# Kernel optimization log

Hardware: AMD Instinct MI355X
Metric: run time of the kernel (lower is better)

The kernel has to match this reference:

```python
import jax, jax.numpy as jnp
import numpy as np

WS = 8          # window_size
HEADS = 6
DH = 32         # dim_head


def _dwconv(t, w):
    # t: (B,C,H,W), w: (C,1,3,3) depthwise, stride 1, padding 1 -> SAME
    return jax.lax.conv_general_dilated(
        t, w, window_strides=(1, 1), padding='SAME',
        feature_group_count=t.shape[1],
        dimension_numbers=('NCHW', 'OIHW', 'NCHW'))


def _l2norm(t, eps=1e-12):
    # matches F.normalize: x / max(||x||, eps)
    n = jnp.sqrt(jnp.sum(t * t, axis=-1, keepdims=True))
    return t / jnp.maximum(n, eps)


def setup_inputs() -> dict:
    key = jax.random.key(0)
    ks = jax.random.split(key, 10)
    B, H, W, C = 2, 256, 256, 192
    s = 0.05
    return {
        'x': jax.random.normal(ks[0], (B, H, W, C), jnp.float32),
        'illu_fea_trans': jax.random.normal(ks[1], (B, H, W, C), jnp.float32),
        'gt_w': jax.random.normal(ks[2], (C, C), jnp.float32) * s,
        'gt_b': jax.random.normal(ks[3], (C,), jnp.float32) * s,
        'qkv_w': jax.random.normal(ks[4], (C, 3 * C), jnp.float32) * s,
        'qkv_b': jax.random.normal(ks[5], (3 * C,), jnp.float32) * s,
        'proj_w': jax.random.normal(ks[6], (C, C), jnp.float32) * s,
        'proj_b': jax.random.normal(ks[7], (C,), jnp.float32) * s,
        'conv1_w': jax.random.normal(ks[8], (C, 1, 3, 3), jnp.float32) * s,
        'conv2_w': jax.random.normal(ks[9], (C, 1, 3, 3), jnp.float32) * s,
    }


def reference(x, illu_fea_trans, gt_w, gt_b, qkv_w, qkv_b, proj_w, proj_b,
              conv1_w, conv2_w):
    B, H, W, C = x.shape
    Ws, heads, d = WS, HEADS, DH
    scale = d ** (-0.5)
    pad_h = (Ws - H % Ws) % Ws
    pad_w = (Ws - W % Ws) % Ws
    xp = jnp.pad(x, ((0, 0), (0, pad_h), (0, pad_w), (0, 0)), mode='reflect')
    ip = jnp.pad(illu_fea_trans, ((0, 0), (0, pad_h), (0, pad_w), (0, 0)), mode='reflect')
    Hp, Wp = xp.shape[1], xp.shape[2]
    nW = (Hp // Ws) * (Wp // Ws)
    T = Ws * Ws

    def to_windows(t):
        t = t.reshape(B, Hp // Ws, Ws, Wp // Ws, Ws, C)
        return t.transpose(0, 1, 3, 2, 4, 5).reshape(B * nW, T, C)

    xw = to_windows(xp)                                  # (B*nW, T, C)
    qkv = (xw @ qkv_w + qkv_b).reshape(B * nW, T, 3, heads, d)
    qkv = qkv.transpose(2, 0, 3, 1, 4)                   # (3, Bn, h, T, d)
    q, k, v = qkv[0], qkv[1], qkv[2]
    q = _l2norm(q)
    k = _l2norm(k)

    illu = to_windows(ip).reshape(B * nW, T, heads, d).transpose(0, 2, 1, 3)
    v = v * (1.0 + jax.nn.sigmoid(illu))

    # global token: avg-pool over padded spatial dims, then linear
    gt = jnp.mean(xp, axis=(1, 2)) @ gt_w + gt_b          # (B, C)
    gt = gt.reshape(B, heads, 1, d)
    # faithful to torch expand(dim=2 -> nW).reshape(B*nW, heads, 1, d)
    gk = jnp.broadcast_to(gt, (B, heads, nW, d)).reshape(B * nW, heads, 1, d)
    k = jnp.concatenate([k, gk], axis=2)                  # (Bn, h, T+1, d)
    v = jnp.concatenate([v, gk], axis=2)

    # chunked softmax over keys == full softmax over key axis (chunks on q only)
    attn = jax.nn.softmax(jnp.einsum('bhqd,bhkd->bhqk', q, k) * scale, axis=-1)
    out = jnp.einsum('bhqk,bhkd->bhqd', attn, v)          # (Bn, h, T, d)
    out = out.transpose(0, 2, 1, 3).reshape(B * nW, T, C)
    out = out @ proj_w + proj_b

    out = out.reshape(B, Hp // Ws, Wp // Ws, Ws, Ws, C)
    out = out.transpose(0, 1, 3, 2, 4, 5).reshape(B, Hp, Wp, C)[:, :H, :W, :]

    # depthwise-conv positional branch on padded x (exact gelu like torch)
    t = xp.transpose(0, 3, 1, 2)                          # (B,C,Hp,Wp)
    t = _dwconv(t, conv1_w)
    t = jax.nn.gelu(t, approximate=False)
    t = _dwconv(t, conv2_w)
    pos = t.transpose(0, 2, 3, 1)[:, :H, :W, :]
    return out + pos
```

## Files before the change

kernel.cpp:

```cpp
#include <hip/hip_runtime.h>
#include <hip/hip_bf16.h>

#define BB   2
#define HH   256
#define WWD  256
#define CC   192
#define WSZ  8
#define TT   64
#define NHD  6
#define DHD  32
#define N3   576

typedef __attribute__((ext_vector_type(8))) short short8;
typedef __attribute__((ext_vector_type(4))) float f32x4;

__device__ inline short bf16_bits(float f) {
  __hip_bfloat16 h = __float2bfloat16(f);
  return __builtin_bit_cast(short, h);
}

__global__ __launch_bounds__(256) void lcam_wshuf(const float* __restrict__ src,
                                                  short* __restrict__ dst,
                                                  int ncols, int nfrag) {
  int gid = blockIdx.x * 256 + threadIdx.x;
  if (gid >= nfrag) return;
  int lane = gid & 63;
  int s = (gid >> 6) % 6;
  int ct = gid / 384;
  int col = ct * 16 + (lane & 15);
  int k0 = s * 32 + (lane >> 4) * 8;
  short8 v;
#pragma unroll
  for (int j = 0; j < 8; ++j)
    v[j] = bf16_bits(src[(size_t)(k0 + j) * ncols + col]);
  *(short8*)(dst + (size_t)gid * 8) = v;
}

__global__ __launch_bounds__(256) void lcam_sum_x(const float* __restrict__ x,
                                                  float* __restrict__ sums) {
  int blk = blockIdx.x;
  int b = blk >> 9;
  int chunk = blk & 511;
  const float* xp = x + ((size_t)b * 65536 + (size_t)chunk * 128) * CC;
  int t = threadIdx.x;
  if (t < CC) {
    float acc = 0.f;
    for (int p = 0; p < 128; ++p) acc += xp[(size_t)p * CC + t];
    atomicAdd(&sums[b * CC + t], acc);
  }
}

__global__ void lcam_gt(const float* __restrict__ sums,
                        const float* __restrict__ gt_w,
                        const float* __restrict__ gt_b,
                        float* __restrict__ gt) {
  int b = blockIdx.x;
  int co = threadIdx.x;
  float acc = gt_b[co];
  const float inv = 1.f / 65536.f;
  for (int c = 0; c < CC; ++c)
    acc += sums[b * CC + c] * inv * gt_w[c * CC + co];
  gt[b * CC + co] = acc;
}

__global__ __launch_bounds__(256) void lcam_attn(
    const float* __restrict__ x, const float* __restrict__ illu,
    const short* __restrict__ wf, const short* __restrict__ pwf,
    const float* __restrict__ qkv_b, const float* __restrict__ proj_b,
    const float* __restrict__ gt, float* __restrict__ out) {
  __shared__ __align__(16) short qs[64 * 40];
  __shared__ __align__(16) short ks[2][65 * 40];
  __shared__ __align__(16) short vt[2][32 * 72];
  __shared__ __align__(16) short ps[64 * 72];
  __shared__ __align__(16) short ot[64 * 40];

  int w = blockIdx.x;
  int b  = w >> 10;
  int wy = (w >> 5) & 31;
  int wx = w & 31;
  int t  = threadIdx.x;
  int lane = t & 63;
  int rtile = t >> 6;
  int m = lane & 15;
  int quad = lane >> 4;
  int key0 = rtile * 16 + quad * 4;

  size_t base = ((size_t)(b * HH + wy * WSZ) * WWD + wx * WSZ) * CC;

  int apix = rtile * 16 + m;
  size_t arow = base + (size_t)((apix >> 3) * WWD + (apix & 7)) * CC + quad * 8;
  short8 afrag[6];
#pragma unroll
  for (int s = 0; s < 6; ++s) {
    const float* ap = x + arow + s * 32;
    float4 f0 = *(const float4*)(ap);
    float4 f1 = *(const float4*)(ap + 4);
    short8 v;
    v[0] = bf16_bits(f0.x); v[1] = bf16_bits(f0.y);
    v[2] = bf16_bits(f0.z); v[3] = bf16_bits(f0.w);
    v[4] = bf16_bits(f1.x); v[5] = bf16_bits(f1.y);
    v[6] = bf16_bits(f1.z); v[7] = bf16_bits(f1.w);
    afrag[s] = v;
  }
  const short8* wf8 = (const short8*)wf;
  const short8* pwf8 = (const short8*)pwf;

  f32x4 pacc[12];
#pragma unroll
  for (int ct = 0; ct < 12; ++ct) {
    f32x4 z = {0.f, 0.f, 0.f, 0.f};
    pacc[ct] = z;
  }

  for (int h = 0; h < NHD; ++h) {
    short* ksb = ks[h & 1];
    short* vtb = vt[h & 1];
    float gv0 = gt[b * CC + h * 32 + m];
    float gv1 = gt[b * CC + h * 32 + 16 + m];
    float il0[4], il1[4];
#pragma unroll
    for (int r = 0; r < 4; ++r) {
      int key = key0 + r;
      const float* ip = illu + base + (size_t)((key >> 3) * WWD + (key & 7)) * CC + h * 32;
      il0[r] = ip[m];
      il1[r] = ip[16 + m];
    }
    {
      f32x4 a0 = {0.f,0.f,0.f,0.f}, a1 = {0.f,0.f,0.f,0.f};
      __builtin_amdgcn_s_setprio(1);
#pragma unroll
      for (int s = 0; s < 6; ++s)
        a0 = __builtin_amdgcn_mfma_f32_16x16x32_bf16(afrag[s], wf8[(2*h)*384 + s*64 + lane], a0, 0,0,0);
#pragma unroll
      for (int s = 0; s < 6; ++s)
        a1 = __builtin_amdgcn_mfma_f32_16x16x32_bf16(afrag[s], wf8[(2*h+1)*384 + s*64 + lane], a1, 0,0,0);
      __builtin_amdgcn_s_setprio(0);
      float b0 = qkv_b[h*32 + m], b1 = qkv_b[h*32 + 16 + m];
#pragma unroll
      for (int r = 0; r < 4; ++r) {
        float v0 = a0[r] + b0, v1 = a1[r] + b1;
        float ss = v0*v0 + v1*v1;
        ss += __shfl_xor(ss, 1); ss += __shfl_xor(ss, 2);
        ss += __shfl_xor(ss, 4); ss += __shfl_xor(ss, 8);
        float scl = 0.17677669529663688f * __builtin_amdgcn_rsqf(fmaxf(ss, 1e-24f));
        int row = key0 + r;
        qs[row*40 + m]      = bf16_bits(v0 * scl);
        qs[row*40 + 16 + m] = bf16_bits(v1 * scl);
      }
    }
    {
      f32x4 a0 = {0.f,0.f,0.f,0.f}, a1 = {0.f,0.f,0.f,0.f};
      __builtin_amdgcn_s_setprio(1);
#pragma unroll
      for (int s = 0; s < 6; ++s)
        a0 = __builtin_amdgcn_mfma_f32_16x16x32_bf16(afrag[s], wf8[(12+2*h)*384 + s*64 + lane], a0, 0,0,0);
#pragma unroll
      for (int s = 0; s < 6; ++s)
        a1 = __builtin_amdgcn_mfma_f32_16x16x32_bf16(afrag[s], wf8[(13+2*h)*384 + s*64 + lane], a1, 0,0,0);
      __builtin_amdgcn_s_setprio(0);
      float b0 = qkv_b[192 + h*32 + m], b1 = qkv_b[192 + h*32 + 16 + m];
#pragma unroll
      for (int r = 0; r < 4; ++r) {
        float v0 = a0[r] + b0, v1 = a1[r] + b1;
        float ss = v0*v0 + v1*v1;
        ss += __shfl_xor(ss, 1); ss += __shfl_xor(ss, 2);
        ss += __shfl_xor(ss, 4); ss += __shfl_xor(ss, 8);
        float scl = __builtin_amdgcn_rsqf(fmaxf(ss, 1e-24f));
        int row = key0 + r;
        ksb[row*40 + m]      = bf16_bits(v0 * scl);
        ksb[row*40 + 16 + m] = bf16_bits(v1 * scl);
      }
    }
    {
      f32x4 a0 = {0.f,0.f,0.f,0.f}, a1 = {0.f,0.f,0.f,0.f};
      __builtin_amdgcn_s_setprio(1);
#pragma unroll
      for (int s = 0; s < 6; ++s)
        a0 = __builtin_amdgcn_mfma_f32_16x16x32_bf16(afrag[s], wf8[(24+2*h)*384 + s*64 + lane], a0, 0,0,0);
#pragma unroll
      for (int s = 0; s < 6; ++s)
        a1 = __builtin_amdgcn_mfma_f32_16x16x32_bf16(afrag[s], wf8[(25+2*h)*384 + s*64 + lane], a1, 0,0,0);
      __builtin_amdgcn_s_setprio(0);
      float b0 = qkv_b[384 + h*32 + m], b1 = qkv_b[384 + h*32 + 16 + m];
#pragma unroll
      for (int r = 0; r < 4; ++r) {
        int key = key0 + r;
        float s0 = __builtin_amdgcn_rcpf(1.f + __expf(-il0[r]));
        float s1 = __builtin_amdgcn_rcpf(1.f + __expf(-il1[r]));
        vtb[m*72 + key]        = bf16_bits((a0[r] + b0) * (1.f + s0));
        vtb[(16 + m)*72 + key] = bf16_bits((a1[r] + b1) * (1.f + s1));
      }
    }
    if (t < DHD) ksb[64*40 + t] = bf16_bits(gt[b*CC + h*DHD + t]);
    __syncthreads();
    short8 qa = *(const short8*)(qs + (rtile*16 + m)*40 + quad*8);
    f32x4 sc[5];
#pragma unroll
    for (int ct = 0; ct < 4; ++ct) {
      short8 kb = *(const short8*)(ksb + (ct*16 + m)*40 + quad*8);
      f32x4 z = {0.f,0.f,0.f,0.f};
      sc[ct] = __builtin_amdgcn_mfma_f32_16x16x32_bf16(qa, kb, z, 0,0,0);
    }
    {
      short8 kb = *(const short8*)(ksb + 64*40 + quad*8);
      f32x4 z = {0.f,0.f,0.f,0.f};
      sc[4] = __builtin_amdgcn_mfma_f32_16x16x32_bf16(qa, kb, z, 0,0,0);
    }
    float p64v[4], invr[4];
#pragma unroll
    for (int r = 0; r < 4; ++r) {
      float e0 = __expf(sc[0][r]), e1 = __expf(sc[1][r]);
      float e2 = __expf(sc[2][r]), e3 = __expf(sc[3][r]);
      float e4 = (m == 0) ? __expf(sc[4][r]) : 0.f;
      int row = key0 + r;
      ps[row*72 + m]      = bf16_bits(e0);
      ps[row*72 + 16 + m] = bf16_bits(e1);
      ps[row*72 + 32 + m] = bf16_bits(e2);
      ps[row*72 + 48 + m] = bf16_bits(e3);
      float sum = e0 + e1 + e2 + e3 + e4;
      sum += __shfl_xor(sum, 1); sum += __shfl_xor(sum, 2);
      sum += __shfl_xor(sum, 4); sum += __shfl_xor(sum, 8);
      invr[r] = __builtin_amdgcn_rcpf(sum);
      p64v[r] = e4;
    }
    f32x4 o0 = {0.f,0.f,0.f,0.f}, o1 = {0.f,0.f,0.f,0.f};
    __builtin_amdgcn_s_setprio(1);
#pragma unroll
    for (int kc = 0; kc < 2; ++kc) {
      short8 pa  = *(const short8*)(ps + (rtile*16 + m)*72 + kc*32 + quad*8);
      short8 vb0 = *(const short8*)(vtb + m*72        + kc*32 + quad*8);
      short8 vb1 = *(const short8*)(vtb + (16 + m)*72 + kc*32 + quad*8);
      o0 = __builtin_amdgcn_mfma_f32_16x16x32_bf16(pa, vb0, o0, 0,0,0);
      o1 = __builtin_amdgcn_mfma_f32_16x16x32_bf16(pa, vb1, o1, 0,0,0);
    }
    __builtin_amdgcn_s_setprio(0);
#pragma unroll
    for (int r = 0; r < 4; ++r) {
      float pr = __shfl(p64v[r], lane & 48);
      int row = key0 + r;
      ot[row*40 + m]      = bf16_bits((o0[r] + pr * gv0) * invr[r]);
      ot[row*40 + 16 + m] = bf16_bits((o1[r] + pr * gv1) * invr[r]);
    }
    short8 oa = *(const short8*)(ot + (rtile*16 + m)*40 + quad*8);
    __builtin_amdgcn_s_setprio(1);
#pragma unroll
    for (int ct = 0; ct < 12; ++ct)
      pacc[ct] = __builtin_amdgcn_mfma_f32_16x16x32_bf16(oa, pwf8[ct*384 + h*64 + lane], pacc[ct], 0,0,0);
    __builtin_amdgcn_s_setprio(0);
  }
#pragma unroll
  for (int ct = 0; ct < 12; ++ct) {
    float bias = proj_b[ct*16 + m];
#pragma unroll
    for (int r = 0; r < 4; ++r) {
      int row = key0 + r;
      out[base + (size_t)((row >> 3) * WWD + (row & 7)) * CC + ct*16 + m] = pacc[ct][r] + bias;
    }
  }
}

__global__ __launch_bounds__(256) void lcam_pos(const float* __restrict__ x,
                                                const float* __restrict__ w1,
                                                const float* __restrict__ w2,
                                                float* __restrict__ out) {
  __shared__ __align__(16) float xt[20 * 20 * 16];
  __shared__ float t1[18 * 18 * 16];
  __shared__ float wl1[16 * 9], wl2[16 * 9];
  int blk = blockIdx.x;
  int cgI = blk % 12; int tmp = blk / 12;
  int tx = tmp % 16; tmp /= 16;
  int ty = tmp % 16; int b = tmp / 16;
  int c0 = cgI * 16;
  int y0 = ty * 16, x0 = tx * 16;
  int t = threadIdx.x;
  if (t < 144) { wl1[t] = w1[c0 * 9 + t]; wl2[t] = w2[c0 * 9 + t]; }
  for (int vi = t; vi < 1600; vi += 256) {
    int cc4 = vi & 3;
    int lin = vi >> 2;
    int xx = lin % 20, yy = lin / 20;
    int gy = y0 - 2 + yy, gx = x0 - 2 + xx;
    float4 v = {0.f, 0.f, 0.f, 0.f};
    if (gy >= 0 && gy < HH && gx >= 0 && gx < WWD)
      v = *(const float4*)(x + (((size_t)b * HH + gy) * WWD + gx) * CC + c0 + cc4 * 4);
    *(float4*)(xt + (yy * 20 + xx) * 16 + cc4 * 4) = v;
  }
  __syncthreads();
  for (int idx = t; idx < 5184; idx += 256) {
    int cc = idx & 15;
    int xx = (idx >> 4) % 18;
    int yy = idx / 288;
    int gy = y0 - 1 + yy, gx = x0 - 1 + xx;
    float r = 0.f;
    if (gy >= 0 && gy < HH && gx >= 0 && gx < WWD) {
#pragma unroll
      for (int ky = 0; ky < 3; ++ky)
#pragma unroll
        for (int kx = 0; kx < 3; ++kx)
          r += xt[((yy + ky) * 20 + xx + kx) * 16 + cc] * wl1[cc * 9 + ky * 3 + kx];
      r = 0.5f * r * (1.f + erff(r * 0.70710678118654752f));
    }
    t1[(yy * 18 + xx) * 16 + cc] = r;
  }
  __syncthreads();
  for (int idx = t; idx < 4096; idx += 256) {
    int cc = idx & 15;
    int xx = (idx >> 4) & 15;
    int yy = idx >> 8;
    float r = 0.f;
#pragma unroll
    for (int ky = 0; ky < 3; ++ky)
#pragma unroll
      for (int kx = 0; kx < 3; ++kx)
        r += t1[((yy + ky) * 18 + xx + kx) * 16 + cc] * wl2[cc * 9 + ky * 3 + kx];
    size_t o = (((size_t)b * HH + y0 + yy) * WWD + x0 + xx) * CC + c0 + cc;
    out[o] += r;
  }
}

extern "C" void kernel_launch(void* const* d_in, const int* in_sizes, int n_in,
                              void* d_out, int out_size, void* d_ws, size_t ws_size,
                              hipStream_t stream) {
  const float* x       = (const float*)d_in[0];
  const float* illu    = (const float*)d_in[1];
  const float* gt_w    = (const float*)d_in[2];
  const float* gt_b    = (const float*)d_in[3];
  const float* qkv_w   = (const float*)d_in[4];
  const float* qkv_b   = (const float*)d_in[5];
  const float* proj_w  = (const float*)d_in[6];
  const float* proj_b  = (const float*)d_in[7];
  const float* conv1_w = (const float*)d_in[8];
  const float* conv2_w = (const float*)d_in[9];
  float* out = (float*)d_out;

  short* wf   = (short*)d_ws;
  short* pwf  = (short*)((char*)d_ws + 221184);
  float* sums = (float*)((char*)d_ws + 221184 + 73728);
  float* gt   = sums + BB * CC;

  hipMemsetAsync(sums, 0, BB * CC * sizeof(float), stream);
  lcam_wshuf<<<54, 256, 0, stream>>>(qkv_w, wf, N3, 36 * 6 * 64);
  lcam_wshuf<<<18, 256, 0, stream>>>(proj_w, pwf, CC, 12 * 6 * 64);
  lcam_sum_x<<<1024, 256, 0, stream>>>(x, sums);
  lcam_gt<<<BB, CC, 0, stream>>>(sums, gt_w, gt_b, gt);
  lcam_attn<<<2048, 256, 0, stream>>>(x, illu, wf, pwf, qkv_b, proj_b, gt, out);
  lcam_pos<<<6144, 256, 0, stream>>>(x, conv1_w, conv2_w, out);
}
```

Measured before the change: 574.7 us.

## Stage per-head QKV and projection weights into LDS via async global_load_lds

The attention kernel now copies each head's QKV weight fragments and projection weight fragments into shared memory with global_load_lds. The next head's QKV weights are prefetched during the softmax stage. The projection weight shuffle is permuted so each head's slice is contiguous. Double-buffered K/V and the separate output buffer are dropped, with qs reused for the output tile and a barrier added at the end of each head. This replaces per-lane global weight reads with LDS reads, but it enlarges shared memory, which may lower occupancy, and adds synchronisation.

```diff
diff --git a/kernel.cpp b/kernel.cpp
--- a/kernel.cpp
+++ b/kernel.cpp
@@ -19,9 +19,15 @@
   return __builtin_bit_cast(short, h);
 }
 
+__device__ inline void stage1k(const short* gsrc, short* ldst, int lane) {
+  __builtin_amdgcn_global_load_lds(
+      (const __attribute__((address_space(1))) void*)(gsrc + lane * 8),
+      (__attribute__((address_space(3))) void*)ldst, 16, 0, 0);
+}
+
 __global__ __launch_bounds__(256) void lcam_wshuf(const float* __restrict__ src,
                                                   short* __restrict__ dst,
-                                                  int ncols, int nfrag) {
+                                                  int ncols, int nfrag, int perm) {
   int gid = blockIdx.x * 256 + threadIdx.x;
   if (gid >= nfrag) return;
   int lane = gid & 63;
@@ -33,7 +39,8 @@
 #pragma unroll
   for (int j = 0; j < 8; ++j)
     v[j] = bf16_bits(src[(size_t)(k0 + j) * ncols + col]);
-  *(short8*)(dst + (size_t)gid * 8) = v;
+  int didx = perm ? ((s * (ncols / 16) + ct) * 64 + lane) : gid;
+  *(short8*)(dst + (size_t)didx * 8) = v;
 }
 
 __global__ __launch_bounds__(256) void lcam_sum_x(const float* __restrict__ x,
@@ -68,11 +75,12 @@
     const short* __restrict__ wf, const short* __restrict__ pwf,
     const float* __restrict__ qkv_b, const float* __restrict__ proj_b,
     const float* __restrict__ gt, float* __restrict__ out) {
+  __shared__ __align__(16) short wq[3 * 768 * 8];
+  __shared__ __align__(16) short wp[768 * 8];
+  __shared__ __align__(16) short ks[65 * 40];
+  __shared__ __align__(16) short vt[32 * 72];
   __shared__ __align__(16) short qs[64 * 40];
-  __shared__ __align__(16) short ks[2][65 * 40];
-  __shared__ __align__(16) short vt[2][32 * 72];
   __shared__ __align__(16) short ps[64 * 72];
-  __shared__ __align__(16) short ot[64 * 40];
 
   int w = blockIdx.x;
   int b  = w >> 10;
@@ -87,6 +95,13 @@
 
   size_t base = ((size_t)(b * HH + wy * WSZ) * WWD + wx * WSZ) * CC;
 
+#pragma unroll
+  for (int u = 0; u < 9; ++u) {
+    int j = rtile * 9 + u;
+    int rr = j / 12, ii = j % 12;
+    stage1k(wf + (rr * 12) * 3072 + ii * 512, wq + rr * 6144 + ii * 512, lane);
+  }
+
   int apix = rtile * 16 + m;
   size_t arow = base + (size_t)((apix >> 3) * WWD + (apix & 7)) * CC + quad * 8;
   short8 afrag[6];
@@ -102,8 +117,8 @@
     v[6] = bf16_bits(f1.z); v[7] = bf16_bits(f1.w);
     afrag[s] = v;
   }
-  const short8* wf8 = (const short8*)wf;
-  const short8* pwf8 = (const short8*)pwf;
+  const short8* wq8 = (const short8*)wq;
+  const short8* wp8 = (const short8*)wp;
 
   f32x4 pacc[12];
 #pragma unroll
@@ -112,9 +127,14 @@
     pacc[ct] = z;
   }
 
+  __syncthreads();
+
   for (int h = 0; h < NHD; ++h) {
-    short* ksb = ks[h & 1];
-    short* vtb = vt[h & 1];
+#pragma unroll
+    for (int u = 0; u < 3; ++u) {
+      int ii = rtile * 3 + u;
+      stage1k(pwf + h * 6144 + ii * 512, wp + ii * 512, lane);
+    }
     float gv0 = gt[b * CC + h * 32 + m];
     float gv1 = gt[b * CC + h * 32 + 16 + m];
     float il0[4], il1[4];
@@ -130,10 +150,10 @@
       __builtin_amdgcn_s_setprio(1);
 #pragma unroll
       for (int s = 0; s < 6; ++s)
-        a0 = __builtin_amdgcn_mfma_f32_16x16x32_bf16(afrag[s], wf8[(2*h)*384 + s*64 + lane], a0, 0,0,0);
-#pragma unroll
-      for (int s = 0; s < 6; ++s)
-        a1 = __builtin_amdgcn_mfma_f32_16x16x32_bf16(afrag[s], wf8[(2*h+1)*384 + s*64 + lane], a1, 0,0,0);
+        a0 = __builtin_amdgcn_mfma_f32_16x16x32_bf16(afrag[s], wq8[s*64 + lane], a0, 0,0,0);
+#pragma unroll
+      for (int s = 0; s < 6; ++s)
+        a1 = __builtin_amdgcn_mfma_f32_16x16x32_bf16(afrag[s], wq8[384 + s*64 + lane], a1, 0,0,0);
       __builtin_amdgcn_s_setprio(0);
       float b0 = qkv_b[h*32 + m], b1 = qkv_b[h*32 + 16 + m];
 #pragma unroll
@@ -153,10 +173,10 @@
       __builtin_amdgcn_s_setprio(1);
 #pragma unroll
       for (int s = 0; s < 6; ++s)
-        a0 = __builtin_amdgcn_mfma_f32_16x16x32_bf16(afrag[s], wf8[(12+2*h)*384 + s*64 + lane], a0, 0,0,0);
-#pragma unroll
-      for (int s = 0; s < 6; ++s)
-        a1 = __builtin_amdgcn_mfma_f32_16x16x32_bf16(afrag[s], wf8[(13+2*h)*384 + s*64 + lane], a1, 0,0,0);
+        a0 = __builtin_amdgcn_mfma_f32_16x16x32_bf16(afrag[s], wq8[768 + s*64 + lane], a0, 0,0,0);
+#pragma unroll
+      for (int s = 0; s < 6; ++s)
+        a1 = __builtin_amdgcn_mfma_f32_16x16x32_bf16(afrag[s], wq8[1152 + s*64 + lane], a1, 0,0,0);
       __builtin_amdgcn_s_setprio(0);
       float b0 = qkv_b[192 + h*32 + m], b1 = qkv_b[192 + h*32 + 16 + m];
 #pragma unroll
@@ -167,8 +187,8 @@
         ss += __shfl_xor(ss, 4); ss += __shfl_xor(ss, 8);
         float scl = __builtin_amdgcn_rsqf(fmaxf(ss, 1e-24f));
         int row = key0 + r;
-        ksb[row*40 + m]      = bf16_bits(v0 * scl);
-        ksb[row*40 + 16 + m] = bf16_bits(v1 * scl);
+        ks[row*40 + m]      = bf16_bits(v0 * scl);
+        ks[row*40 + 16 + m] = bf16_bits(v1 * scl);
       }
     }
     {
@@ -176,10 +196,10 @@
       __builtin_amdgcn_s_setprio(1);
 #pragma unroll
       for (int s = 0; s < 6; ++s)
-        a0 = __builtin_amdgcn_mfma_f32_16x16x32_bf16(afrag[s], wf8[(24+2*h)*384 + s*64 + lane], a0, 0,0,0);
-#pragma unroll
-      for (int s = 0; s < 6; ++s)
-        a1 = __builtin_amdgcn_mfma_f32_16x16x32_bf16(afrag[s], wf8[(25+2*h)*384 + s*64 + lane], a1, 0,0,0);
+        a0 = __builtin_amdgcn_mfma_f32_16x16x32_bf16(afrag[s], wq8[1536 + s*64 + lane], a0, 0,0,0);
+#pragma unroll
+      for (int s = 0; s < 6; ++s)
+        a1 = __builtin_amdgcn_mfma_f32_16x16x32_bf16(afrag[s], wq8[1920 + s*64 + lane], a1, 0,0,0);
       __builtin_amdgcn_s_setprio(0);
       float b0 = qkv_b[384 + h*32 + m], b1 = qkv_b[384 + h*32 + 16 + m];
 #pragma unroll
@@ -187,24 +207,33 @@
         int key = key0 + r;
         float s0 = __builtin_amdgcn_rcpf(1.f + __expf(-il0[r]));
         float s1 = __builtin_amdgcn_rcpf(1.f + __expf(-il1[r]));
-        vtb[m*72 + key]        = bf16_bits((a0[r] + b0) * (1.f + s0));
-        vtb[(16 + m)*72 + key] = bf16_bits((a1[r] + b1) * (1.f + s1));
+        vt[m*72 + key]        = bf16_bits((a0[r] + b0) * (1.f + s0));
+        vt[(16 + m)*72 + key] = bf16_bits((a1[r] + b1) * (1.f + s1));
       }
     }
-    if (t < DHD) ksb[64*40 + t] = bf16_bits(gt[b*CC + h*DHD + t]);
+    if (t < DHD) ks[64*40 + t] = bf16_bits(gt[b*CC + h*DHD + t]);
     __syncthreads();
     short8 qa = *(const short8*)(qs + (rtile*16 + m)*40 + quad*8);
     f32x4 sc[5];
 #pragma unroll
     for (int ct = 0; ct < 4; ++ct) {
-      short8 kb = *(const short8*)(ksb + (ct*16 + m)*40 + quad*8);
+      short8 kb = *(const short8*)(ks + (ct*16 + m)*40 + quad*8);
       f32x4 z = {0.f,0.f,0.f,0.f};
       sc[ct] = __builtin_amdgcn_mfma_f32_16x16x32_bf16(qa, kb, z, 0,0,0);
     }
     {
-      short8 kb = *(const short8*)(ksb + 64*40 + quad*8);
+      short8 kb = *(const short8*)(ks + 64*40 + quad*8);
       f32x4 z = {0.f,0.f,0.f,0.f};
       sc[4] = __builtin_amdgcn_mfma_f32_16x16x32_bf16(qa, kb, z, 0,0,0);
+    }
+    if (h < NHD - 1) {
+#pragma unroll
+      for (int u = 0; u < 9; ++u) {
+        int j = rtile * 9 + u;
+        int rr = j / 12, ii = j % 12;
+        stage1k(wf + (rr * 12 + 2 * (h + 1)) * 3072 + ii * 512,
+                wq + rr * 6144 + ii * 512, lane);
+      }
     }
     float p64v[4], invr[4];
 #pragma unroll
@@ -228,8 +257,8 @@
 #pragma unroll
     for (int kc = 0; kc < 2; ++kc) {
       short8 pa  = *(const short8*)(ps + (rtile*16 + m)*72 + kc*32 + quad*8);
-      short8 vb0 = *(const short8*)(vtb + m*72        + kc*32 + quad*8);
-      short8 vb1 = *(const short8*)(vtb + (16 + m)*72 + kc*32 + quad*8);
+      short8 vb0 = *(const short8*)(vt + m*72        + kc*32 + quad*8);
+      short8 vb1 = *(const short8*)(vt + (16 + m)*72 + kc*32 + quad*8);
       o0 = __builtin_amdgcn_mfma_f32_16x16x32_bf16(pa, vb0, o0, 0,0,0);
       o1 = __builtin_amdgcn_mfma_f32_16x16x32_bf16(pa, vb1, o1, 0,0,0);
     }
@@ -238,15 +267,16 @@
     for (int r = 0; r < 4; ++r) {
       float pr = __shfl(p64v[r], lane & 48);
       int row = key0 + r;
-      ot[row*40 + m]      = bf16_bits((o0[r] + pr * gv0) * invr[r]);
-      ot[row*40 + 16 + m] = bf16_bits((o1[r] + pr * gv1) * invr[r]);
-    }
-    short8 oa = *(const short8*)(ot + (rtile*16 + m)*40 + quad*8);
+      qs[row*40 + m]      = bf16_bits((o0[r] + pr * gv0) * invr[r]);
+      qs[row*40 + 16 + m] = bf16_bits((o1[r] + pr * gv1) * invr[r]);
+    }
+    short8 oa = *(const short8*)(qs + (rtile*16 + m)*40 + quad*8);
     __builtin_amdgcn_s_setprio(1);
 #pragma unroll
     for (int ct = 0; ct < 12; ++ct)
-      pacc[ct] = __builtin_amdgcn_mfma_f32_16x16x32_bf16(oa, pwf8[ct*384 + h*64 + lane], pacc[ct], 0,0,0);
+      pacc[ct] = __builtin_amdgcn_mfma_f32_16x16x32_bf16(oa, wp8[ct*64 + lane], pacc[ct], 0,0,0);
     __builtin_amdgcn_s_setprio(0);
+    __syncthreads();
   }
 #pragma unroll
   for (int ct = 0; ct < 12; ++ct) {
@@ -338,8 +368,8 @@
   float* gt   = sums + BB * CC;
 
   hipMemsetAsync(sums, 0, BB * CC * sizeof(float), stream);
-  lcam_wshuf<<<54, 256, 0, stream>>>(qkv_w, wf, N3, 36 * 6 * 64);
-  lcam_wshuf<<<18, 256, 0, stream>>>(proj_w, pwf, CC, 12 * 6 * 64);
+  lcam_wshuf<<<54, 256, 0, stream>>>(qkv_w, wf, N3, 36 * 6 * 64, 0);
+  lcam_wshuf<<<18, 256, 0, stream>>>(proj_w, pwf, CC, 12 * 6 * 64, 1);
   lcam_sum_x<<<1024, 256, 0, stream>>>(x, sums);
   lcam_gt<<<BB, CC, 0, stream>>>(sums, gt_w, gt_b, gt);
   lcam_attn<<<2048, 256, 0, stream>>>(x, illu, wf, pwf, qkv_b, proj_b, gt, out);
```

Result: faster. 501.9 us (-12.7%).
